# Kernel tuning notes

Hardware: AMD Instinct MI355X
Metric: run time of the kernel (lower is better)

## Reference

```python
import jax, jax.numpy as jnp
import numpy as np

D_MODEL = 1024
D_KEY = 64
N_HEADS = 16
B, T = 4, 2048


def setup_inputs() -> dict:
    key = jax.random.key(0)
    ks = jax.random.split(key, 12)
    s = 0.02
    return {
        "keys": jax.random.normal(ks[0], (B, T, D_MODEL), jnp.float32),
        "queries": jax.random.normal(ks[1], (B, T, D_MODEL), jnp.float32),
        "values": jax.random.normal(ks[2], (B, T, D_MODEL), jnp.float32),
        "pad_mask": jnp.ones((B, T), jnp.int32),
        "WK_w": jax.random.normal(ks[3], (D_KEY * N_HEADS, D_MODEL), jnp.float32) * s,
        "WK_b": jnp.zeros((D_KEY * N_HEADS,), jnp.float32),
        "WQ_w": jax.random.normal(ks[4], (D_KEY * N_HEADS, D_MODEL), jnp.float32) * s,
        "WQ_b": jnp.zeros((D_KEY * N_HEADS,), jnp.float32),
        "WV_w": jax.random.normal(ks[5], (D_KEY * N_HEADS, D_MODEL), jnp.float32) * s,
        "WV_b": jnp.zeros((D_KEY * N_HEADS,), jnp.float32),
        "WO_w": jax.random.normal(ks[6], (D_MODEL, D_KEY * N_HEADS), jnp.float32) * s,
        "WO_b": jnp.zeros((D_MODEL,), jnp.float32),
    }


def reference(keys, queries, values, pad_mask, WK_w, WK_b, WQ_w, WQ_b, WV_w, WV_b, WO_w, WO_b):
    # NOTE: the original torch module calls masked_fill (non-inplace) and discards
    # the result, so neither the causal mask nor pad_mask has any effect. We
    # faithfully reproduce that: no masking. pad_mask is an unused constant.
    batch, time = keys.shape[:2]
    k = keys @ WK_w.T + WK_b      # [B,T,H*dk]
    q = queries @ WQ_w.T + WQ_b
    v = values @ WV_w.T + WV_b

    def split_heads(x):
        return x.reshape(batch, time, N_HEADS, D_KEY).transpose(0, 2, 1, 3)  # [B,H,T,dk]

    k, q, v = split_heads(k), split_heads(q), split_heads(v)
    # scores[t,s] = k_t . q_s / sqrt(d_key)  (K and Q swapped, as in source)
    scores = jnp.einsum("bhtd,bhsd->bhts", k, q) / jnp.sqrt(jnp.float32(D_KEY))
    attn = jax.nn.softmax(scores, axis=-1)             # [B,H,T,T]
    ctx = jnp.einsum("bhts,bhsd->bhtd", attn, v)       # [B,H,T,dk]
    ctx = ctx.transpose(0, 2, 1, 3).reshape(batch, time, N_HEADS * D_KEY)
    return ctx @ WO_w.T + WO_b
```

## Files before the change

### kernel.cpp

```cpp
#include <hip/hip_runtime.h>

typedef unsigned short u16;
typedef unsigned int u32;
typedef __attribute__((ext_vector_type(8))) short short8;
typedef __attribute__((ext_vector_type(4))) float f32x4;

__device__ __forceinline__ u16 f2bf(float f) {
    unsigned int u = __float_as_uint(f);
    u += 0x7fffu + ((u >> 16) & 1u);
    return (u16)(u >> 16);
}

__device__ __forceinline__ u32 pack_trunc(float a, float b) {
    return __builtin_amdgcn_perm(__float_as_uint(b), __float_as_uint(a), 0x07060302u);
}

__device__ __forceinline__ void gload16(const u16* g, const u16* l) {
    __builtin_amdgcn_global_load_lds(
        (const __attribute__((address_space(1))) unsigned int*)g,
        (__attribute__((address_space(3))) unsigned int*)l, 16, 0, 0);
}

__global__ __launch_bounds__(256) void cast_all(const float* __restrict__ k,
                                                const float* __restrict__ q,
                                                const float* __restrict__ v,
                                                const float* __restrict__ wk,
                                                const float* __restrict__ wq,
                                                const float* __restrict__ wv,
                                                const float* __restrict__ wo,
                                                u16* __restrict__ Xk, u16* __restrict__ Xq,
                                                u16* __restrict__ Xv, u16* __restrict__ Wk,
                                                u16* __restrict__ Wq, u16* __restrict__ Wv,
                                                u16* __restrict__ Wo) {
    size_t i = ((size_t)blockIdx.x * 256 + threadIdx.x) * 8;
    const float* src; u16* dst; size_t off;
    if (i < 25165824) {
        int r = (int)(i >> 23); off = i & 8388607;
        src = r == 0 ? k : (r == 1 ? q : v);
        dst = r == 0 ? Xk : (r == 1 ? Xq : Xv);
    } else {
        size_t j = i - 25165824;
        int r = (int)(j >> 20); off = j & 1048575;
        src = r == 0 ? wk : (r == 1 ? wq : (r == 2 ? wv : wo));
        dst = r == 0 ? Wk : (r == 1 ? Wq : (r == 2 ? Wv : Wo));
    }
    float4 a = *(const float4*)(src + off);
    float4 b = *(const float4*)(src + off + 4);
    union { u16 h[8]; uint4 u; } r8;
    r8.h[0] = f2bf(a.x); r8.h[1] = f2bf(a.y); r8.h[2] = f2bf(a.z); r8.h[3] = f2bf(a.w);
    r8.h[4] = f2bf(b.x); r8.h[5] = f2bf(b.y); r8.h[6] = f2bf(b.z); r8.h[7] = f2bf(b.w);
    *(uint4*)(dst + off) = r8.u;
}


__global__ __launch_bounds__(256) void gemm_qkv(const u16* __restrict__ Xk,
                                                const u16* __restrict__ Xq,
                                                const u16* __restrict__ Xv,
                                                const u16* __restrict__ Wk,
                                                const u16* __restrict__ Wq,
                                                const u16* __restrict__ Wv,
                                                const float* __restrict__ bK,
                                                const float* __restrict__ bQ,
                                                const float* __restrict__ bV,
                                                u16* __restrict__ Kbh,
                                                u16* __restrict__ Qbh,
                                                u16* __restrict__ Vtg,
                                                float kscale) {
    __shared__ u16 sA[128 * 64];
    __shared__ u16 sB[128 * 64];
    const int f = blockIdx.x;
    const int z = f >> 9;
    const int r9 = f & 511;
    const int i_idx = (r9 & 7) | (((r9 >> 6) & 7) << 3);
    const int j_idx = (r9 >> 3) & 7;

    const u16* X = z == 0 ? Xk : (z == 1 ? Xq : Xv);
    const u16* W = z == 0 ? Wk : (z == 1 ? Wq : Wv);
    const float* bias = z == 0 ? bK : (z == 1 ? bQ : bV);
    u16* out = z == 0 ? Kbh : (z == 1 ? Qbh : Vtg);
    const float scale = z == 0 ? kscale : 1.0f;

    const int tid  = threadIdx.x;
    const int wave = tid >> 6, lane = tid & 63;
    const int quad = lane >> 4, l16 = lane & 15;
    const int wm = wave & 1, wn = wave >> 1;
    const int i0 = i_idx * 128, j0 = j_idx * 128;

    const int r = tid >> 3;
    const int sg = (tid & 7) ^ (r & 7);
    const u16* gA = X + (size_t)(i0 + r) * 1024 + sg * 8;
    const u16* gB = W + (size_t)(j0 + r) * 1024 + sg * 8;
    u16* dA = sA + wave * 512;
    u16* dB = sB + wave * 512;
    const int sx = l16 & 7;

    f32x4 acc[4][4];
    #pragma unroll
    for (int mt = 0; mt < 4; mt++)
        #pragma unroll
        for (int nt = 0; nt < 4; nt++) acc[mt][nt] = (f32x4){0.f, 0.f, 0.f, 0.f};

    for (int kk = 0; kk < 1024; kk += 64) {
        __syncthreads();
        gload16(gA + kk,         dA);
        gload16(gA + kk + 32768, dA + 2048);
        gload16(gA + kk + 65536, dA + 4096);
        gload16(gA + kk + 98304, dA + 6144);
        gload16(gB + kk,         dB);
        gload16(gB + kk + 32768, dB + 2048);
        gload16(gB + kk + 65536, dB + 4096);
        gload16(gB + kk + 98304, dB + 6144);
        __syncthreads();
        short8 bf[4][2];
        #pragma unroll
        for (int nt = 0; nt < 4; nt++)
            #pragma unroll
            for (int kh = 0; kh < 2; kh++)
                bf[nt][kh] = *(const short8*)&sB[(wn * 64 + nt * 16 + l16) * 64 +
                                                 ((kh * 4 + quad) ^ sx) * 8];
        #pragma unroll
        for (int mt = 0; mt < 4; mt++) {
            const int arow = (wm * 64 + mt * 16 + l16) * 64;
            short8 a0 = *(const short8*)&sA[arow + ((quad) ^ sx) * 8];
            short8 a1 = *(const short8*)&sA[arow + ((4 + quad) ^ sx) * 8];
            #pragma unroll
            for (int nt = 0; nt < 4; nt++) {
                acc[mt][nt] = __builtin_amdgcn_mfma_f32_16x16x32_bf16(a0, bf[nt][0], acc[mt][nt], 0, 0, 0);
                acc[mt][nt] = __builtin_amdgcn_mfma_f32_16x16x32_bf16(a1, bf[nt][1], acc[mt][nt], 0, 0, 0);
            }
        }
    }

    #pragma unroll
    for (int mt = 0; mt < 4; mt++) {
        #pragma unroll
        for (int nt = 0; nt < 4; nt++) {
            int j = j0 + wn * 64 + nt * 16 + l16;
            float bj = bias[j];
            #pragma unroll
            for (int rr = 0; rr < 4; rr++) {
                int i = i0 + wm * 64 + mt * 16 + quad * 4 + rr;
                float v = (acc[mt][nt][rr] + bj) * scale;
                int b = i >> 11, t = i & 2047;
                int h = j >> 6,  dd = j & 63;
                size_t idx;
                if (z == 2) idx = (((size_t)(b * 16 + h)) * 64 + dd) * 2048 + t;
                else        idx = (((size_t)(b * 16 + h)) * 2048 + t) * 64 + dd;
                out[idx] = f2bf(v);
            }
        }
    }
}

__global__ __launch_bounds__(256) void gemm_out(const u16* __restrict__ X,
                                                const u16* __restrict__ W,
                                                const float* __restrict__ bias,
                                                float* __restrict__ out) {
    __shared__ u16 sA[128 * 64];
    __shared__ u16 sB[64 * 64];
    const int f = blockIdx.x;
    const int j_idx = (f >> 3) & 15;
    const int i_idx = (f & 7) | ((f >> 7) << 3);
    const int tid  = threadIdx.x;
    const int wave = tid >> 6, lane = tid & 63;
    const int quad = lane >> 4, l16 = lane & 15;
    const int wm = wave & 1, wn = wave >> 1;
    const int i0 = i_idx * 128, j0 = j_idx * 64;

    const int r = tid >> 3;
    const int sg = (tid & 7) ^ (r & 7);
    const u16* gA = X + (size_t)(i0 + r) * 1024 + sg * 8;
    const u16* gB = W + (size_t)(j0 + r) * 1024 + sg * 8;
    u16* dA = sA + wave * 512;
    u16* dB = sB + wave * 512;
    const int sx = l16 & 7;

    f32x4 acc[4][2];
    #pragma unroll
    for (int mt = 0; mt < 4; mt++) {
        acc[mt][0] = (f32x4){0.f, 0.f, 0.f, 0.f};
        acc[mt][1] = (f32x4){0.f, 0.f, 0.f, 0.f};
    }

    for (int kk = 0; kk < 1024; kk += 64) {
        __syncthreads();
        gload16(gA + kk,         dA);
        gload16(gA + kk + 32768, dA + 2048);
        gload16(gA + kk + 65536, dA + 4096);
        gload16(gA + kk + 98304, dA + 6144);
        gload16(gB + kk,         dB);
        gload16(gB + kk + 32768, dB + 2048);
        __syncthreads();
        short8 bf[2][2];
        #pragma unroll
        for (int nt = 0; nt < 2; nt++)
            #pragma unroll
            for (int kh = 0; kh < 2; kh++)
                bf[nt][kh] = *(const short8*)&sB[(wn * 32 + nt * 16 + l16) * 64 +
                                                 ((kh * 4 + quad) ^ sx) * 8];
        #pragma unroll
        for (int mt = 0; mt < 4; mt++) {
            const int arow = (wm * 64 + mt * 16 + l16) * 64;
            short8 a0 = *(const short8*)&sA[arow + ((quad) ^ sx) * 8];
            short8 a1 = *(const short8*)&sA[arow + ((4 + quad) ^ sx) * 8];
            #pragma unroll
            for (int nt = 0; nt < 2; nt++) {
                acc[mt][nt] = __builtin_amdgcn_mfma_f32_16x16x32_bf16(a0, bf[nt][0], acc[mt][nt], 0, 0, 0);
                acc[mt][nt] = __builtin_amdgcn_mfma_f32_16x16x32_bf16(a1, bf[nt][1], acc[mt][nt], 0, 0, 0);
            }
        }
    }

    #pragma unroll
    for (int mt = 0; mt < 4; mt++) {
        #pragma unroll
        for (int nt = 0; nt < 2; nt++) {
            int j = j0 + wn * 32 + nt * 16 + l16;
            float bj = bias[j];
            #pragma unroll
            for (int rr = 0; rr < 4; rr++) {
                int i = i0 + wm * 64 + mt * 16 + quad * 4 + rr;
                out[(size_t)i * 1024 + j] = acc[mt][nt][rr] + bj;
            }
        }
    }
}

#define QST 72

__global__ __launch_bounds__(256, 2) void attn_kernel(const u16* __restrict__ Kbh,
                                                      const u16* __restrict__ Qbh,
                                                      const u16* __restrict__ Vtg,
                                                      u16* __restrict__ ctx) {
    __shared__ u16 sQ[64 * QST];
    __shared__ u16 sVt[64 * QST];
    __shared__ u16 sP[4 * 2 * 16 * QST];
    const int f = blockIdx.x;
    const int bh = (f & 7) | ((f >> 6) << 3);
    const int tx = (f >> 3) & 7;
    const int tid  = threadIdx.x;
    const int wave = tid >> 6, lane = tid & 63;
    const int quad = lane >> 4, l16 = lane & 15;
    const int t0 = tx * 256;
    const int tw = t0 + wave * 64;
    const size_t base = (size_t)bh * 2048 * 64;

    short8 bk[4][2];
    #pragma unroll
    for (int g = 0; g < 4; g++) {
        const u16* kr = Kbh + base + (size_t)(tw + g * 16 + l16) * 64 + quad * 8;
        bk[g][0] = *(const short8*)kr;
        bk[g][1] = *(const short8*)(kr + 32);
    }
    const short8 ones = {0x3F80, 0x3F80, 0x3F80, 0x3F80, 0x3F80, 0x3F80, 0x3F80, 0x3F80};

    f32x4 accO[4][4];
    #pragma unroll
    for (int g = 0; g < 4; g++)
        #pragma unroll
        for (int dt = 0; dt < 4; dt++) accO[g][dt] = (f32x4){0.f, 0.f, 0.f, 0.f};
    f32x4 accL[4];
    #pragma unroll
    for (int g = 0; g < 4; g++) accL[g] = (f32x4){0.f, 0.f, 0.f, 0.f};

    const int srow = tid >> 2, seg = tid & 3;
    u16* sPw = sP + wave * 2 * 16 * QST;

    for (int s0 = 0; s0 < 2048; s0 += 64) {
        __syncthreads();
        {
            const uint4* gq = (const uint4*)(Qbh + base + (size_t)(s0 + srow) * 64 + seg * 16);
            uint4 q0 = gq[0], q1 = gq[1];
            *(uint4*)&sQ[srow * QST + seg * 16]     = q0;
            *(uint4*)&sQ[srow * QST + seg * 16 + 8] = q1;
        }
        {
            const uint4* gv = (const uint4*)(Vtg + ((size_t)bh * 64 + srow) * 2048 + s0 + seg * 16);
            uint4 v0 = gv[0], v1 = gv[1];
            *(uint4*)&sVt[srow * QST + seg * 16]     = v0;
            *(uint4*)&sVt[srow * QST + seg * 16 + 8] = v1;
        }
        __syncthreads();

        short8 aq[4][2], av[2][4];
        #pragma unroll
        for (int nt = 0; nt < 4; nt++) {
            aq[nt][0] = *(const short8*)&sQ[(nt * 16 + l16) * QST + quad * 8];
            aq[nt][1] = *(const short8*)&sQ[(nt * 16 + l16) * QST + 32 + quad * 8];
        }
        #pragma unroll
        for (int kk = 0; kk < 2; kk++)
            #pragma unroll
            for (int dt = 0; dt < 4; dt++)
                av[kk][dt] = *(const short8*)&sVt[(dt * 16 + l16) * QST + kk * 32 + quad * 8];

        #pragma unroll
        for (int g = 0; g < 4; g++) {
            f32x4 aS[4];
            #pragma unroll
            for (int nt = 0; nt < 4; nt++) {
                f32x4 s = __builtin_amdgcn_mfma_f32_16x16x32_bf16(aq[nt][0], bk[g][0],
                            (f32x4){0.f, 0.f, 0.f, 0.f}, 0, 0, 0);
                aS[nt] = __builtin_amdgcn_mfma_f32_16x16x32_bf16(aq[nt][1], bk[g][1], s, 0, 0, 0);
            }
            u16* pb = sPw + (g & 1) * 16 * QST;
            #pragma unroll
            for (int nt = 0; nt < 4; nt++) {
                float p0 = __builtin_amdgcn_exp2f(aS[nt][0]);
                float p1 = __builtin_amdgcn_exp2f(aS[nt][1]);
                float p2 = __builtin_amdgcn_exp2f(aS[nt][2]);
                float p3 = __builtin_amdgcn_exp2f(aS[nt][3]);
                uint2 pk = { pack_trunc(p0, p1), pack_trunc(p2, p3) };
                *(uint2*)&pb[l16 * QST + nt * 16 + quad * 4] = pk;
            }
            #pragma unroll
            for (int kk = 0; kk < 2; kk++) {
                short8 bp = *(const short8*)&pb[l16 * QST + kk * 32 + quad * 8];
                accL[g] = __builtin_amdgcn_mfma_f32_16x16x32_bf16(ones, bp, accL[g], 0, 0, 0);
                #pragma unroll
                for (int dt = 0; dt < 4; dt++)
                    accO[g][dt] = __builtin_amdgcn_mfma_f32_16x16x32_bf16(av[kk][dt], bp, accO[g][dt], 0, 0, 0);
            }
        }
    }

    const int b = bh >> 4, h = bh & 15;
    #pragma unroll
    for (int g = 0; g < 4; g++) {
        float inv = 1.f / accL[g][0];
        int t = tw + g * 16 + l16;
        u16* orow = ctx + ((size_t)(b * 2048 + t)) * 1024 + h * 64;
        #pragma unroll
        for (int dt = 0; dt < 4; dt++) {
            union { u16 h4[4]; uint2 u; } o;
            #pragma unroll
            for (int rr = 0; rr < 4; rr++) o.h4[rr] = f2bf(accO[g][dt][rr] * inv);
            *(uint2*)&orow[dt * 16 + quad * 4] = o.u;
        }
    }
}

extern "C" void kernel_launch(void* const* d_in, const int* in_sizes, int n_in,
                              void* d_out, int out_size, void* d_ws, size_t ws_size,
                              hipStream_t stream) {
    const float* keys    = (const float*)d_in[0];
    const float* queries = (const float*)d_in[1];
    const float* values  = (const float*)d_in[2];
    const float* WKb = (const float*)d_in[5];
    const float* WQb = (const float*)d_in[7];
    const float* WVb = (const float*)d_in[9];
    const float* WOb = (const float*)d_in[11];

    char* ws = (char*)d_ws;
    const size_t MB = 1 << 20;
    u16* Kbh = (u16*)(ws + 0 * MB);
    u16* Qbh = (u16*)(ws + 16 * MB);
    u16* Vtg = (u16*)(ws + 32 * MB);
    u16* Xk  = (u16*)(ws + 48 * MB);
    u16* Xq  = (u16*)(ws + 64 * MB);
    u16* Xv  = (u16*)(ws + 80 * MB);
    u16* Wk  = (u16*)(ws + 96 * MB);
    u16* Wq  = (u16*)(ws + 98 * MB);
    u16* Wv  = (u16*)(ws + 100 * MB);
    u16* Wo  = (u16*)(ws + 102 * MB);
    u16* ctx = (u16*)(ws + 48 * MB);

    cast_all<<<14336, 256, 0, stream>>>(keys, queries, values,
                                        (const float*)d_in[4], (const float*)d_in[6],
                                        (const float*)d_in[8], (const float*)d_in[10],
                                        Xk, Xq, Xv, Wk, Wq, Wv, Wo);

    const float kscale = 1.4426950408889634f * 0.125f;
    gemm_qkv<<<1536, 256, 0, stream>>>(Xk, Xq, Xv, Wk, Wq, Wv,
                                       WKb, WQb, WVb, Kbh, Qbh, Vtg, kscale);

    attn_kernel<<<512, 256, 0, stream>>>(Kbh, Qbh, Vtg, ctx);

    gemm_out<<<1024, 256, 0, stream>>>(ctx, Wo, WOb, (float*)d_out);
}
```

Measured before the change: 334.9 us.

## Halve attention rows per block, swizzle LDS tiles, add MFMA priority hints

Each attention block now covers 128 query rows instead of 256 (32 per wave), so the grid doubles to 1024 blocks and launch bounds rise to 4 blocks per CU for better occupancy. LDS padding (stride 72) is replaced by an XOR swizzle on 64-wide rows for the Q, V and P tiles, which shrinks shared memory while still avoiding bank conflicts. s_setprio is raised around the MFMA sections so they get issue priority over other waves. The trade-off is that each Q/V tile load is now shared by fewer rows, which doubles the global and LDS staging traffic per unit of compute.

```diff
diff --git a/kernel.cpp b/kernel.cpp
--- a/kernel.cpp
+++ b/kernel.cpp
@@ -226,84 +226,89 @@
     }
 }
 
-#define QST 72
-
-__global__ __launch_bounds__(256, 2) void attn_kernel(const u16* __restrict__ Kbh,
+__global__ __launch_bounds__(256, 4) void attn_kernel(const u16* __restrict__ Kbh,
                                                       const u16* __restrict__ Qbh,
                                                       const u16* __restrict__ Vtg,
                                                       u16* __restrict__ ctx) {
-    __shared__ u16 sQ[64 * QST];
-    __shared__ u16 sVt[64 * QST];
-    __shared__ u16 sP[4 * 2 * 16 * QST];
+    __shared__ u16 sQ[64 * 64];
+    __shared__ u16 sVt[64 * 64];
+    __shared__ u16 sP[4 * 2 * 16 * 64];
     const int f = blockIdx.x;
-    const int bh = (f & 7) | ((f >> 6) << 3);
-    const int tx = (f >> 3) & 7;
+    const int bh = (f & 7) | ((f >> 7) << 3);
+    const int tx = (f >> 3) & 15;
     const int tid  = threadIdx.x;
     const int wave = tid >> 6, lane = tid & 63;
     const int quad = lane >> 4, l16 = lane & 15;
-    const int t0 = tx * 256;
-    const int tw = t0 + wave * 64;
+    const int sx = l16 & 7;
+    const int tw = tx * 128 + wave * 32;
     const size_t base = (size_t)bh * 2048 * 64;
 
-    short8 bk[4][2];
-    #pragma unroll
-    for (int g = 0; g < 4; g++) {
+    short8 bk[2][2];
+    #pragma unroll
+    for (int g = 0; g < 2; g++) {
         const u16* kr = Kbh + base + (size_t)(tw + g * 16 + l16) * 64 + quad * 8;
         bk[g][0] = *(const short8*)kr;
         bk[g][1] = *(const short8*)(kr + 32);
     }
     const short8 ones = {0x3F80, 0x3F80, 0x3F80, 0x3F80, 0x3F80, 0x3F80, 0x3F80, 0x3F80};
 
-    f32x4 accO[4][4];
-    #pragma unroll
-    for (int g = 0; g < 4; g++)
+    f32x4 accO[2][4];
+    #pragma unroll
+    for (int g = 0; g < 2; g++)
         #pragma unroll
         for (int dt = 0; dt < 4; dt++) accO[g][dt] = (f32x4){0.f, 0.f, 0.f, 0.f};
-    f32x4 accL[4];
-    #pragma unroll
-    for (int g = 0; g < 4; g++) accL[g] = (f32x4){0.f, 0.f, 0.f, 0.f};
+    f32x4 accL[2];
+    accL[0] = (f32x4){0.f, 0.f, 0.f, 0.f};
+    accL[1] = (f32x4){0.f, 0.f, 0.f, 0.f};
 
     const int srow = tid >> 2, seg = tid & 3;
-    u16* sPw = sP + wave * 2 * 16 * QST;
+    const int s7 = srow & 7;
+    const int st0 = ((2 * seg)     ^ s7) * 8;
+    const int st1 = ((2 * seg + 1) ^ s7) * 8;
+    u16* sPw = sP + wave * 2048;
 
     for (int s0 = 0; s0 < 2048; s0 += 64) {
         __syncthreads();
         {
             const uint4* gq = (const uint4*)(Qbh + base + (size_t)(s0 + srow) * 64 + seg * 16);
             uint4 q0 = gq[0], q1 = gq[1];
-            *(uint4*)&sQ[srow * QST + seg * 16]     = q0;
-            *(uint4*)&sQ[srow * QST + seg * 16 + 8] = q1;
+            *(uint4*)&sQ[srow * 64 + st0] = q0;
+            *(uint4*)&sQ[srow * 64 + st1] = q1;
         }
         {
             const uint4* gv = (const uint4*)(Vtg + ((size_t)bh * 64 + srow) * 2048 + s0 + seg * 16);
             uint4 v0 = gv[0], v1 = gv[1];
-            *(uint4*)&sVt[srow * QST + seg * 16]     = v0;
-            *(uint4*)&sVt[srow * QST + seg * 16 + 8] = v1;
+            *(uint4*)&sVt[srow * 64 + st0] = v0;
+            *(uint4*)&sVt[srow * 64 + st1] = v1;
         }
         __syncthreads();
 
         short8 aq[4][2], av[2][4];
         #pragma unroll
-        for (int nt = 0; nt < 4; nt++) {
-            aq[nt][0] = *(const short8*)&sQ[(nt * 16 + l16) * QST + quad * 8];
-            aq[nt][1] = *(const short8*)&sQ[(nt * 16 + l16) * QST + 32 + quad * 8];
-        }
+        for (int nt = 0; nt < 4; nt++)
+            #pragma unroll
+            for (int kh = 0; kh < 2; kh++)
+                aq[nt][kh] = *(const short8*)&sQ[(nt * 16 + l16) * 64 +
+                                                 ((kh * 4 + quad) ^ sx) * 8];
         #pragma unroll
         for (int kk = 0; kk < 2; kk++)
             #pragma unroll
             for (int dt = 0; dt < 4; dt++)
-                av[kk][dt] = *(const short8*)&sVt[(dt * 16 + l16) * QST + kk * 32 + quad * 8];
-
-        #pragma unroll
-        for (int g = 0; g < 4; g++) {
+                av[kk][dt] = *(const short8*)&sVt[(dt * 16 + l16) * 64 +
+                                                  ((kk * 4 + quad) ^ sx) * 8];
+
+        #pragma unroll
+        for (int g = 0; g < 2; g++) {
             f32x4 aS[4];
+            __builtin_amdgcn_s_setprio(1);
             #pragma unroll
             for (int nt = 0; nt < 4; nt++) {
                 f32x4 s = __builtin_amdgcn_mfma_f32_16x16x32_bf16(aq[nt][0], bk[g][0],
                             (f32x4){0.f, 0.f, 0.f, 0.f}, 0, 0, 0);
                 aS[nt] = __builtin_amdgcn_mfma_f32_16x16x32_bf16(aq[nt][1], bk[g][1], s, 0, 0, 0);
             }
-            u16* pb = sPw + (g & 1) * 16 * QST;
+            __builtin_amdgcn_s_setprio(0);
+            u16* pb = sPw + (g & 1) * 1024;
             #pragma unroll
             for (int nt = 0; nt < 4; nt++) {
                 float p0 = __builtin_amdgcn_exp2f(aS[nt][0]);
@@ -311,22 +316,25 @@
                 float p2 = __builtin_amdgcn_exp2f(aS[nt][2]);
                 float p3 = __builtin_amdgcn_exp2f(aS[nt][3]);
                 uint2 pk = { pack_trunc(p0, p1), pack_trunc(p2, p3) };
-                *(uint2*)&pb[l16 * QST + nt * 16 + quad * 4] = pk;
-            }
+                *(uint2*)&pb[l16 * 64 + ((nt * 4 + quad) ^ (sx << 1)) * 4] = pk;
+            }
+            __builtin_amdgcn_s_setprio(1);
             #pragma unroll
             for (int kk = 0; kk < 2; kk++) {
-                short8 bp = *(const short8*)&pb[l16 * QST + kk * 32 + quad * 8];
+                short8 bp = *(const short8*)&pb[l16 * 64 +
+                                                ((kk * 8 + quad * 2) ^ (sx << 1)) * 4];
                 accL[g] = __builtin_amdgcn_mfma_f32_16x16x32_bf16(ones, bp, accL[g], 0, 0, 0);
                 #pragma unroll
                 for (int dt = 0; dt < 4; dt++)
                     accO[g][dt] = __builtin_amdgcn_mfma_f32_16x16x32_bf16(av[kk][dt], bp, accO[g][dt], 0, 0, 0);
             }
+            __builtin_amdgcn_s_setprio(0);
         }
     }
 
     const int b = bh >> 4, h = bh & 15;
     #pragma unroll
-    for (int g = 0; g < 4; g++) {
+    for (int g = 0; g < 2; g++) {
         float inv = 1.f / accL[g][0];
         int t = tw + g * 16 + l16;
         u16* orow = ctx + ((size_t)(b * 2048 + t)) * 1024 + h * 64;
@@ -374,7 +382,7 @@
     gemm_qkv<<<1536, 256, 0, stream>>>(Xk, Xq, Xv, Wk, Wq, Wv,
                                        WKb, WQb, WVb, Kbh, Qbh, Vtg, kscale);
 
-    attn_kernel<<<512, 256, 0, stream>>>(Kbh, Qbh, Vtg, ctx);
+    attn_kernel<<<1024, 256, 0, stream>>>(Kbh, Qbh, Vtg, ctx);
 
     gemm_out<<<1024, 256, 0, stream>>>(ctx, Wo, WOb, (float*)d_out);
 }
```

Measured after the change: 508.1 us. 1.52x slower.
